# Optimization experiments

Measured on AMD Instinct MI355X. Metric: run time of the kernel, lower is better.

Reference implementation:

```python
import jax, jax.numpy as jnp
import numpy as np

EPS = 1e-5
LOSS_WEIGHT = 0.3
IGNORE_INDEX = -100


def rmsnorm(x, w):
    # x: (B,S,D), w: (D,)
    var = jnp.mean(x * x, axis=-1, keepdims=True)
    return x * jax.lax.rsqrt(var + EPS) * w


def cross_entropy(logits, targets):
    # logits: (B,T,V), targets: (B,T) int; ignore_index=-100, mean reduction
    logp = jax.nn.log_softmax(logits, axis=-1)
    valid = targets != IGNORE_INDEX
    safe_t = jnp.where(valid, targets, 0)
    nll = -jnp.take_along_axis(logp, safe_t[..., None], axis=-1)[..., 0]
    nll = jnp.where(valid, nll, 0.0)
    return jnp.sum(nll) / jnp.maximum(jnp.sum(valid), 1)


def setup_inputs() -> dict:
    key = jax.random.key(0)
    ks = jax.random.split(key, 5)
    B, S, D, V, H = 1, 2048, 1024, 50257, 3
    hidden = jax.random.normal(ks[0], (B, S, D), dtype=jnp.float32)
    targets = jax.random.randint(ks[1], (B, S), 0, V, dtype=jnp.int64)
    emb_w = jax.random.normal(ks[2], (V, D), dtype=jnp.float32) * 0.02
    main_norm_w = jnp.ones((D,), dtype=jnp.float32)
    aux_proj_w = jax.random.normal(ks[3], (H - 1, D, D), dtype=jnp.float32) * 0.02
    aux_norm_w = jnp.ones((H - 1, D), dtype=jnp.float32)
    aux_out_w = jax.random.normal(ks[4], (H - 1, V, D), dtype=jnp.float32) * 0.02
    return {"hidden": hidden, "targets": targets, "emb_w": emb_w,
            "main_norm_w": main_norm_w, "aux_proj_w": aux_proj_w,
            "aux_norm_w": aux_norm_w, "aux_out_w": aux_out_w}


def reference(hidden, targets, emb_w, main_norm_w, aux_proj_w, aux_norm_w, aux_out_w):
    # Main head: norm -> tied vocab projection
    main_logits = jnp.einsum('bsd,vd->bsv', rmsnorm(hidden, main_norm_w), emb_w)
    main_loss = cross_entropy(main_logits[:, :-1, :], targets[:, 1:])

    # Auxiliary heads predict t+2, t+3, ...
    n_aux = aux_proj_w.shape[0]
    aux_losses = []
    for i in range(n_aux):
        k = i + 2
        h = jnp.einsum('bsd,ed->bse', hidden, aux_proj_w[i])  # d_model -> d_model
        logits = jnp.einsum('bsd,vd->bsv', rmsnorm(h, aux_norm_w[i]), aux_out_w[i])
        aux_losses.append(cross_entropy(logits[:, :-k, :], targets[:, k:]))
    total_aux = sum(aux_losses) / len(aux_losses) if aux_losses else jnp.float32(0.0)
    loss = main_loss + LOSS_WEIGHT * total_aux
    return main_logits, loss
```

## Files before the change

kernel.cpp:

```cpp
#include <hip/hip_runtime.h>
#include <hip/hip_bf16.h>


typedef __hip_bfloat16 bf16;
typedef __attribute__((ext_vector_type(8))) short bf16x8;
typedef __attribute__((ext_vector_type(4))) float f32x4;

typedef const __attribute__((address_space(1))) void* gptr_t;
typedef __attribute__((address_space(3))) void* lptr_t;

#define S_LEN   2048
#define DMODEL  1024
#define VOCAB   50257
#define VPAD2   51200
#define NT256   200

__device__ __forceinline__ void gload_lds16(const void* g, void* l) {
  __builtin_amdgcn_global_load_lds((gptr_t)g, (lptr_t)l, 16, 0, 0);
}

__global__ __launch_bounds__(256) void k_cvt(const float* __restrict__ src,
                                             bf16* __restrict__ dst,
                                             long rows_src, long rows_pad) {
  const long total4 = rows_pad << 8;
  for (long i = (long)blockIdx.x * 256 + threadIdx.x; i < total4;
       i += (long)gridDim.x * 256) {
    const long e = i << 2;
    const long row = e >> 10;
    alignas(8) bf16 o[4];
    if (row < rows_src) {
      const float4 v = *(const float4*)(src + e);
      o[0] = __float2bfloat16(v.x); o[1] = __float2bfloat16(v.y);
      o[2] = __float2bfloat16(v.z); o[3] = __float2bfloat16(v.w);
    } else {
      o[0] = o[1] = o[2] = o[3] = __float2bfloat16(0.f);
    }
    *(uint2*)(dst + e) = *(const uint2*)o;
  }
}

__global__ __launch_bounds__(256) void k_rms(const float* __restrict__ x,
                                             const float* __restrict__ w,
                                             bf16* __restrict__ xn) {
  const int row = blockIdx.x;
  const int t = threadIdx.x;
  const float4 v = ((const float4*)(x + (size_t)row * DMODEL))[t];
  float ss = v.x*v.x + v.y*v.y + v.z*v.z + v.w*v.w;
  #pragma unroll
  for (int d = 1; d < 64; d <<= 1) ss += __shfl_xor(ss, d, 64);
  __shared__ float red[4];
  if ((t & 63) == 0) red[t >> 6] = ss;
  __syncthreads();
  const float tot = red[0] + red[1] + red[2] + red[3];
  const float scale = rsqrtf(tot * (1.f / DMODEL) + 1e-5f);
  const float4 wv = ((const float4*)w)[t];
  alignas(8) bf16 o[4];
  o[0] = __float2bfloat16(v.x * scale * wv.x);
  o[1] = __float2bfloat16(v.y * scale * wv.y);
  o[2] = __float2bfloat16(v.z * scale * wv.z);
  o[3] = __float2bfloat16(v.w * scale * wv.w);
  *(uint2*)(xn + (size_t)row * DMODEL + t * 4) = *(const uint2*)o;
}

template<bool WRITE_OUT, bool DO_CE>
__global__ __launch_bounds__(512, 2)
void k_gemm256(const bf16* __restrict__ A, const bf16* __restrict__ B,
               float* __restrict__ C, long ldc, int Nvalid,
               const int* __restrict__ targets, int shift,
               float* __restrict__ pmax, float* __restrict__ psum,
               float* __restrict__ ptgt, int ntiles) {
  __shared__ char lds[131072 + 9216];

  const int t = threadIdx.x;
  const int w = t >> 6, l = t & 63;
  const int g = l >> 4, q = l & 15;
  const int wr = w >> 2, wc = w & 3;
  const int id = blockIdx.x;
  const int bm = (id >> 3) & 7;
  const int bn = (id & 7) + ((id >> 6) << 3);

  f32x4 acc[8][4];
  #pragma unroll
  for (int i = 0; i < 8; ++i)
    #pragma unroll
    for (int j = 0; j < 4; ++j)
      #pragma unroll
      for (int r = 0; r < 4; ++r) acc[i][j][r] = 0.f;

  const int srow = (l >> 2);
  const int scol = ((l & 3) * 8) ^ (((l >> 5) & 1) * 16);
  const char* gA0 = (const char*)(A + (size_t)(bm * 256 + (w * 2 + 0) * 16 + srow) * DMODEL + scol);
  const char* gA1 = (const char*)(A + (size_t)(bm * 256 + (w * 2 + 1) * 16 + srow) * DMODEL + scol);
  const char* gB0 = (const char*)(B + (size_t)(bn * 256 + (w * 2 + 0) * 16 + srow) * DMODEL + scol);
  const char* gB1 = (const char*)(B + (size_t)(bn * 256 + (w * 2 + 1) * 16 + srow) * DMODEL + scol);

  const int laneoff = (q * 64 + g * 16) ^ (((q >> 3) & 1) << 5);
  const char* rdA = lds + wr * 8192 + laneoff;
  const char* rdB = lds + 16384 + wc * 4096 + laneoff;

#define RDA(BUF, KK, MI) (*(const bf16x8*)(rdA + (BUF)*65536 + (KK)*32768 + (MI)*1024))
#define RDB(BUF, KK, NI) (*(const bf16x8*)(rdB + (BUF)*65536 + (KK)*32768 + (NI)*1024))

#define STAGE(BUF, H, KOFF) do {                                                  \
    char* lb_ = lds + (BUF)*65536 + ((H)>>1)*32768 + ((H)&1)*16384 + w * 2048;    \
    const char* s0_ = ((H)&1) ? gB0 : gA0;                                        \
    const char* s1_ = ((H)&1) ? gB1 : gA1;                                        \
    gload_lds16(s0_ + (KOFF) + ((H)>>1)*64, lb_);                                 \
    gload_lds16(s1_ + (KOFF) + ((H)>>1)*64, lb_ + 1024);                          \
  } while (0)

#define PH_MFMA(MH)                                                               \
    __builtin_amdgcn_s_barrier();                                                 \
    __builtin_amdgcn_s_setprio(1);                                                \
    _Pragma("unroll")                                                             \
    for (int mi_ = 0; mi_ < 4; ++mi_)                                             \
      _Pragma("unroll")                                                           \
      for (int ni_ = 0; ni_ < 4; ++ni_)                                           \
        acc[(MH)*4 + mi_][ni_] = __builtin_amdgcn_mfma_f32_16x16x32_bf16(         \
            a[mi_], b[ni_], acc[(MH)*4 + mi_][ni_], 0, 0, 0);                     \
    __builtin_amdgcn_s_setprio(0);

#define TILE(BUF, DOSTG, KOFF, LAST) do {                                         \
    bf16x8 a[4], b[4];                                                            \
    _Pragma("unroll") for (int mi_ = 0; mi_ < 4; ++mi_) a[mi_] = RDA(BUF, 0, mi_);\
    _Pragma("unroll") for (int ni_ = 0; ni_ < 4; ++ni_) b[ni_] = RDB(BUF, 0, ni_);\
    if (DOSTG) STAGE(1-(BUF), 0, KOFF);                                           \
    PH_MFMA(0)                                                                    \
    __builtin_amdgcn_s_barrier();                                                 \
    _Pragma("unroll") for (int mi_ = 0; mi_ < 4; ++mi_) a[mi_] = RDA(BUF, 0, 4+mi_);\
    if (DOSTG) STAGE(1-(BUF), 1, KOFF);                                           \
    PH_MFMA(1)                                                                    \
    if (DOSTG) { asm volatile("s_waitcnt vmcnt(4)" ::: "memory"); }               \
    if (LAST)  { asm volatile("s_waitcnt vmcnt(0)" ::: "memory"); }               \
    __builtin_amdgcn_s_barrier();                                                 \
    _Pragma("unroll") for (int mi_ = 0; mi_ < 4; ++mi_) a[mi_] = RDA(BUF, 1, mi_);\
    _Pragma("unroll") for (int ni_ = 0; ni_ < 4; ++ni_) b[ni_] = RDB(BUF, 1, ni_);\
    if (DOSTG) STAGE(1-(BUF), 2, KOFF);                                           \
    PH_MFMA(0)                                                                    \
    __builtin_amdgcn_s_barrier();                                                 \
    _Pragma("unroll") for (int mi_ = 0; mi_ < 4; ++mi_) a[mi_] = RDA(BUF, 1, 4+mi_);\
    if (DOSTG) STAGE(1-(BUF), 3, KOFF);                                           \
    PH_MFMA(1)                                                                    \
    if (DOSTG) { asm volatile("s_waitcnt vmcnt(4)" ::: "memory"); }               \
    __builtin_amdgcn_s_barrier();                                                 \
  } while (0)

  STAGE(0, 0, 0); STAGE(0, 1, 0); STAGE(0, 2, 0); STAGE(0, 3, 0);
  asm volatile("s_waitcnt vmcnt(4)" ::: "memory");
  __builtin_amdgcn_s_barrier();

  for (int t2 = 0; t2 < 7; ++t2) {
    TILE(0, 1, 128, 0);
    TILE(1, 1, 256, 0);
    gA0 += 256; gA1 += 256; gB0 += 256; gB1 += 256;
  }
  TILE(0, 1, 128, 0);
  TILE(1, 0, 0, 1);

#undef TILE
#undef PH_MFMA
#undef STAGE
#undef RDA
#undef RDB

  if constexpr (WRITE_OUT) {
    #pragma unroll
    for (int mi = 0; mi < 8; ++mi) {
      #pragma unroll
      for (int r = 0; r < 4; ++r) {
        const long row = bm * 256 + wr * 128 + mi * 16 + g * 4 + r;
        #pragma unroll
        for (int ni = 0; ni < 4; ++ni) {
          const int col = bn * 256 + wc * 64 + ni * 16 + q;
          if (col < Nvalid) C[row * ldc + col] = acc[mi][ni][r];
        }
      }
    }
  }

  if constexpr (DO_CE) {
    float* lds_m = (float*)(lds + 131072);
    float* lds_s = lds_m + 1024;
    int* lds_tgt = (int*)(lds_s + 1024);
    if (t < 256) {
      const int rowg = bm * 256 + t;
      lds_tgt[t] = (rowg < S_LEN - shift) ? targets[rowg + shift] : -1;
    }
    __syncthreads();
    #pragma unroll
    for (int mi = 0; mi < 8; ++mi) {
      #pragma unroll
      for (int r = 0; r < 4; ++r) {
        const int rl = wr * 128 + mi * 16 + g * 4 + r;
        const int tgt = lds_tgt[rl];
        float v[4];
        #pragma unroll
        for (int ni = 0; ni < 4; ++ni) {
          const int n = bn * 256 + wc * 64 + ni * 16 + q;
          const float av = acc[mi][ni][r];
          if (n == tgt) ptgt[bm * 256 + rl] = av;
          v[ni] = (n < Nvalid) ? av : -1e30f;
        }
        float m = fmaxf(fmaxf(v[0], v[1]), fmaxf(v[2], v[3]));
        #pragma unroll
        for (int d = 1; d < 16; d <<= 1) m = fmaxf(m, __shfl_xor(m, d, 64));
        float s = 0.f;
        #pragma unroll
        for (int ni = 0; ni < 4; ++ni) s += __expf(v[ni] - m);
        #pragma unroll
        for (int d = 1; d < 16; d <<= 1) s += __shfl_xor(s, d, 64);
        if (q == 0) { lds_m[rl * 4 + wc] = m; lds_s[rl * 4 + wc] = s; }
      }
    }
    __syncthreads();
    if (t < 256) {
      float M = lds_m[t * 4 + 0], Ssum = lds_s[t * 4 + 0];
      #pragma unroll
      for (int c = 1; c < 4; ++c) {
        const float m2 = lds_m[t * 4 + c], s2 = lds_s[t * 4 + c];
        const float nM = fmaxf(M, m2);
        Ssum = Ssum * __expf(M - nM) + s2 * __expf(m2 - nM);
        M = nM;
      }
      const size_t idx = (size_t)(bm * 256 + t) * ntiles + bn;
      pmax[idx] = M;
      psum[idx] = Ssum;
    }
  }
}

__global__ __launch_bounds__(256, 2)
void k_gemm(const bf16* __restrict__ A, const bf16* __restrict__ B,
            float* __restrict__ C, long ldc, int Nvalid) {
  constexpr int K = DMODEL;
  __shared__ bf16 As[128 * 32];
  __shared__ bf16 Bs[128 * 32];

  const int t = threadIdx.x;
  const int bn = blockIdx.x, bm = blockIdx.y;
  const int w = t >> 6, l = t & 63, g = l >> 4, q = l & 15;
  const int wr = w >> 1, wc = w & 1;

  f32x4 acc[4][4];
  #pragma unroll
  for (int i = 0; i < 4; ++i)
    #pragma unroll
    for (int j = 0; j < 4; ++j)
      #pragma unroll
      for (int r = 0; r < 4; ++r) acc[i][j][r] = 0.f;

  char* lA0 = (char*)As + w * 1024;
  char* lA1 = (char*)As + 4096 + w * 1024;
  char* lB0 = (char*)Bs + w * 1024;
  char* lB1 = (char*)Bs + 4096 + w * 1024;
  const char* gA0 = (const char*)(A + (size_t)(bm * 128 + (t >> 2)) * K) + (t & 3) * 16;
  const char* gA1 = gA0 + (size_t)64 * K * 2;
  const char* gB0 = (const char*)(B + (size_t)(bn * 128 + (t >> 2)) * K) + (t & 3) * 16;
  const char* gB1 = gB0 + (size_t)64 * K * 2;

  for (int k0 = 0; k0 < K; k0 += 32) {
    const int kb = k0 * 2;
    gload_lds16(gA0 + kb, lA0);
    gload_lds16(gA1 + kb, lA1);
    gload_lds16(gB0 + kb, lB0);
    gload_lds16(gB1 + kb, lB1);
    __syncthreads();
    bf16x8 a[4], b[4];
    #pragma unroll
    for (int mi = 0; mi < 4; ++mi)
      a[mi] = *(const bf16x8*)&As[(wr * 64 + mi * 16 + q) * 32 + g * 8];
    #pragma unroll
    for (int ni = 0; ni < 4; ++ni)
      b[ni] = *(const bf16x8*)&Bs[(wc * 64 + ni * 16 + q) * 32 + g * 8];
    #pragma unroll
    for (int mi = 0; mi < 4; ++mi)
      #pragma unroll
      for (int ni = 0; ni < 4; ++ni)
        acc[mi][ni] = __builtin_amdgcn_mfma_f32_16x16x32_bf16(a[mi], b[ni], acc[mi][ni], 0, 0, 0);
    __syncthreads();
  }

  #pragma unroll
  for (int mi = 0; mi < 4; ++mi) {
    #pragma unroll
    for (int r = 0; r < 4; ++r) {
      const long row = bm * 128 + wr * 64 + mi * 16 + g * 4 + r;
      #pragma unroll
      for (int ni = 0; ni < 4; ++ni) {
        const int col = bn * 128 + wc * 64 + ni * 16 + q;
        if (col < Nvalid) C[row * ldc + col] = acc[mi][ni][r];
      }
    }
  }
}

__global__ __launch_bounds__(64) void k_combine(const float* __restrict__ pmax,
                                                const float* __restrict__ psum,
                                                const float* __restrict__ ptgt,
                                                float* __restrict__ nll,
                                                int ntiles, int nv) {
  const int r = blockIdx.x;
  const int l = threadIdx.x;
  float M = -1e30f, Ssum = 0.f;
  for (int tl = l; tl < ntiles; tl += 64) {
    const float m = pmax[(size_t)r * ntiles + tl];
    const float s = psum[(size_t)r * ntiles + tl];
    const float nM = fmaxf(M, m);
    Ssum = Ssum * __expf(M - nM) + s * __expf(m - nM);
    M = nM;
  }
  #pragma unroll
  for (int d = 1; d < 64; d <<= 1) {
    const float m2 = __shfl_xor(M, d, 64);
    const float s2 = __shfl_xor(Ssum, d, 64);
    const float nM = fmaxf(M, m2);
    Ssum = Ssum * __expf(M - nM) + s2 * __expf(m2 - nM);
    M = nM;
  }
  if (l == 0) nll[r] = (r < nv) ? (M + logf(Ssum) - ptgt[r]) : 0.f;
}

__global__ __launch_bounds__(256) void k_loss(const float* __restrict__ nll,
                                              float* __restrict__ out) {
  __shared__ float sh[256];
  const int t = threadIdx.x;
  float sums[3];
  #pragma unroll
  for (int h = 0; h < 3; ++h) {
    const int nv = 2047 - h;
    float s = 0.f;
    for (int r = t; r < nv; r += 256) s += nll[h * 2048 + r];
    sh[t] = s; __syncthreads();
    for (int off = 128; off > 0; off >>= 1) {
      if (t < off) sh[t] += sh[t + off];
      __syncthreads();
    }
    sums[h] = sh[0]; __syncthreads();
  }
  if (t == 0)
    out[0] = sums[0] / 2047.f + 0.3f * 0.5f * (sums[1] / 2046.f + sums[2] / 2045.f);
}

extern "C" void kernel_launch(void* const* d_in, const int* in_sizes, int n_in,
                              void* d_out, int out_size, void* d_ws, size_t ws_size,
                              hipStream_t stream) {
  const float* hidden      = (const float*)d_in[0];
  const int*   targets     = (const int*)d_in[1];
  const float* emb_w       = (const float*)d_in[2];
  const float* main_norm_w = (const float*)d_in[3];
  const float* aux_proj_w  = (const float*)d_in[4];
  const float* aux_norm_w  = (const float*)d_in[5];
  const float* aux_out_w   = (const float*)d_in[6];
  float* out = (float*)d_out;

  char* ws = (char*)d_ws;
  bf16*  Wb    = (bf16*)(ws);
  bf16*  hb    = (bf16*)(ws + 104857600);
  bf16*  xn    = (bf16*)(ws + 109051904);
  bf16*  projb = (bf16*)(ws + 113246208);
  float* hbuf  = (float*)(ws + 117440512);
  float* pmax  = (float*)(ws + 125829120);
  float* psum  = (float*)(ws + 127467520);
  float* ptgt  = (float*)(ws + 129105920);
  float* nll   = (float*)(ws + 129114112);

  k_cvt<<<2048, 256, 0, stream>>>(hidden, hb, 2048, 2048);
  k_cvt<<<2048, 256, 0, stream>>>(aux_proj_w, projb, 2048, 2048);
  k_rms<<<2048, 256, 0, stream>>>(hidden, main_norm_w, xn);

  k_cvt<<<2048, 256, 0, stream>>>(emb_w, Wb, VOCAB, VPAD2);
  k_gemm256<true, true><<<1600, 512, 0, stream>>>(
      xn, Wb, out, VOCAB, VOCAB, targets, 1, pmax, psum, ptgt, NT256);
  k_combine<<<2048, 64, 0, stream>>>(pmax, psum, ptgt, nll, NT256, 2047);

  for (int i = 0; i < 2; ++i) {
    k_cvt<<<2048, 256, 0, stream>>>(aux_out_w + (size_t)i * VOCAB * DMODEL, Wb, VOCAB, VPAD2);
    k_gemm<<<dim3(8, 16), 256, 0, stream>>>(
        hb, projb + (size_t)i * DMODEL * DMODEL, hbuf, DMODEL, DMODEL);
    k_rms<<<2048, 256, 0, stream>>>(hbuf, aux_norm_w + (size_t)i * DMODEL, xn);
    k_gemm256<false, true><<<1600, 512, 0, stream>>>(
        xn, Wb, nullptr, 0, VOCAB, targets, i + 2, pmax, psum, ptgt, NT256);
    k_combine<<<2048, 64, 0, stream>>>(pmax, psum, ptgt, nll + (i + 1) * 2048, NT256, 2048 - (i + 2));
  }

  k_loss<<<1, 256, 0, stream>>>(nll, out + (size_t)S_LEN * VOCAB);
}
```

Before: 1.205 ms.

## Replace double-buffered GEMM loop with multi-slot ring pipeline, per-head slot counts

```diff
diff --git a/kernel.cpp b/kernel.cpp
--- a/kernel.cpp
+++ b/kernel.cpp
@@ -62,14 +62,14 @@
   *(uint2*)(xn + (size_t)row * DMODEL + t * 4) = *(const uint2*)o;
 }
 
-template<bool WRITE_OUT, bool DO_CE>
+template<int SLOTS, bool WRITE_OUT, bool DO_CE>
 __global__ __launch_bounds__(512, 2)
 void k_gemm256(const bf16* __restrict__ A, const bf16* __restrict__ B,
                float* __restrict__ C, long ldc, int Nvalid,
                const int* __restrict__ targets, int shift,
                float* __restrict__ pmax, float* __restrict__ psum,
                float* __restrict__ ptgt, int ntiles) {
-  __shared__ char lds[131072 + 9216];
+  __shared__ char lds[SLOTS * 32768 + 9216];
 
   const int t = threadIdx.x;
   const int w = t >> 6, l = t & 63;
@@ -89,79 +89,83 @@
 
   const int srow = (l >> 2);
   const int scol = ((l & 3) * 8) ^ (((l >> 5) & 1) * 16);
-  const char* gA0 = (const char*)(A + (size_t)(bm * 256 + (w * 2 + 0) * 16 + srow) * DMODEL + scol);
-  const char* gA1 = (const char*)(A + (size_t)(bm * 256 + (w * 2 + 1) * 16 + srow) * DMODEL + scol);
-  const char* gB0 = (const char*)(B + (size_t)(bn * 256 + (w * 2 + 0) * 16 + srow) * DMODEL + scol);
-  const char* gB1 = (const char*)(B + (size_t)(bn * 256 + (w * 2 + 1) * 16 + srow) * DMODEL + scol);
+  const char* gA0 = (const char*)(A + (size_t)(bm * 256 + w * 32 + srow) * DMODEL + scol);
+  const char* gA1 = gA0 + (size_t)16 * DMODEL * 2;
+  const char* gB0 = (const char*)(B + (size_t)(bn * 256 + w * 32 + srow) * DMODEL + scol);
+  const char* gB1 = gB0 + (size_t)16 * DMODEL * 2;
 
   const int laneoff = (q * 64 + g * 16) ^ (((q >> 3) & 1) << 5);
   const char* rdA = lds + wr * 8192 + laneoff;
   const char* rdB = lds + 16384 + wc * 4096 + laneoff;
 
-#define RDA(BUF, KK, MI) (*(const bf16x8*)(rdA + (BUF)*65536 + (KK)*32768 + (MI)*1024))
-#define RDB(BUF, KK, NI) (*(const bf16x8*)(rdB + (BUF)*65536 + (KK)*32768 + (NI)*1024))
-
-#define STAGE(BUF, H, KOFF) do {                                                  \
-    char* lb_ = lds + (BUF)*65536 + ((H)>>1)*32768 + ((H)&1)*16384 + w * 2048;    \
-    const char* s0_ = ((H)&1) ? gB0 : gA0;                                        \
-    const char* s1_ = ((H)&1) ? gB1 : gA1;                                        \
-    gload_lds16(s0_ + (KOFF) + ((H)>>1)*64, lb_);                                 \
-    gload_lds16(s1_ + (KOFF) + ((H)>>1)*64, lb_ + 1024);                          \
-  } while (0)
-
-#define PH_MFMA(MH)                                                               \
-    __builtin_amdgcn_s_barrier();                                                 \
-    __builtin_amdgcn_s_setprio(1);                                                \
-    _Pragma("unroll")                                                             \
-    for (int mi_ = 0; mi_ < 4; ++mi_)                                             \
-      _Pragma("unroll")                                                           \
-      for (int ni_ = 0; ni_ < 4; ++ni_)                                           \
-        acc[(MH)*4 + mi_][ni_] = __builtin_amdgcn_mfma_f32_16x16x32_bf16(         \
-            a[mi_], b[ni_], acc[(MH)*4 + mi_][ni_], 0, 0, 0);                     \
+  auto lda = [&](int s, int mi) {
+    return *(const bf16x8*)(rdA + s * 32768 + mi * 1024);
+  };
+  auto ldb = [&](int s, int ni) {
+    return *(const bf16x8*)(rdB + s * 32768 + ni * 1024);
+  };
+  auto stageA = [&](int s, int koff) {
+    char* lb = lds + s * 32768 + w * 2048;
+    gload_lds16(gA0 + koff, lb);
+    gload_lds16(gA1 + koff, lb + 1024);
+  };
+  auto stageB = [&](int s, int koff) {
+    char* lb = lds + s * 32768 + 16384 + w * 2048;
+    gload_lds16(gB0 + koff, lb);
+    gload_lds16(gB1 + koff, lb + 1024);
+  };
+
+  #pragma unroll
+  for (int p = 0; p < SLOTS - 1; ++p) { stageA(p, p * 64); stageB(p, p * 64); }
+  if constexpr (SLOTS == 4) asm volatile("s_waitcnt vmcnt(8)" ::: "memory");
+  else if constexpr (SLOTS == 3) asm volatile("s_waitcnt vmcnt(4)" ::: "memory");
+  else asm volatile("s_waitcnt vmcnt(0)" ::: "memory");
+  __builtin_amdgcn_s_barrier();
+
+  #pragma unroll
+  for (int j = 0; j < 32; ++j) {
+    const int s = j % SLOTS;
+    const int sp = (j + SLOTS - 1) % SLOTS;
+    const int koff = (j + SLOTS - 1) * 64;
+    const bool do_stage = (j + SLOTS - 1) < 32;
+    bf16x8 a[4], b[4];
+
+    #pragma unroll
+    for (int mi = 0; mi < 4; ++mi) a[mi] = lda(s, mi);
+    #pragma unroll
+    for (int ni = 0; ni < 4; ++ni) b[ni] = ldb(s, ni);
+    if (do_stage) stageA(sp, koff);
+    __builtin_amdgcn_s_barrier();
+    __builtin_amdgcn_s_setprio(1);
+    #pragma unroll
+    for (int mi = 0; mi < 4; ++mi)
+      #pragma unroll
+      for (int ni = 0; ni < 4; ++ni)
+        acc[mi][ni] = __builtin_amdgcn_mfma_f32_16x16x32_bf16(a[mi], b[ni], acc[mi][ni], 0, 0, 0);
     __builtin_amdgcn_s_setprio(0);
-
-#define TILE(BUF, DOSTG, KOFF, LAST) do {                                         \
-    bf16x8 a[4], b[4];                                                            \
-    _Pragma("unroll") for (int mi_ = 0; mi_ < 4; ++mi_) a[mi_] = RDA(BUF, 0, mi_);\
-    _Pragma("unroll") for (int ni_ = 0; ni_ < 4; ++ni_) b[ni_] = RDB(BUF, 0, ni_);\
-    if (DOSTG) STAGE(1-(BUF), 0, KOFF);                                           \
-    PH_MFMA(0)                                                                    \
-    __builtin_amdgcn_s_barrier();                                                 \
-    _Pragma("unroll") for (int mi_ = 0; mi_ < 4; ++mi_) a[mi_] = RDA(BUF, 0, 4+mi_);\
-    if (DOSTG) STAGE(1-(BUF), 1, KOFF);                                           \
-    PH_MFMA(1)                                                                    \
-    if (DOSTG) { asm volatile("s_waitcnt vmcnt(4)" ::: "memory"); }               \
-    if (LAST)  { asm volatile("s_waitcnt vmcnt(0)" ::: "memory"); }               \
-    __builtin_amdgcn_s_barrier();                                                 \
-    _Pragma("unroll") for (int mi_ = 0; mi_ < 4; ++mi_) a[mi_] = RDA(BUF, 1, mi_);\
-    _Pragma("unroll") for (int ni_ = 0; ni_ < 4; ++ni_) b[ni_] = RDB(BUF, 1, ni_);\
-    if (DOSTG) STAGE(1-(BUF), 2, KOFF);                                           \
-    PH_MFMA(0)                                                                    \
-    __builtin_amdgcn_s_barrier();                                                 \
-    _Pragma("unroll") for (int mi_ = 0; mi_ < 4; ++mi_) a[mi_] = RDA(BUF, 1, 4+mi_);\
-    if (DOSTG) STAGE(1-(BUF), 3, KOFF);                                           \
-    PH_MFMA(1)                                                                    \
-    if (DOSTG) { asm volatile("s_waitcnt vmcnt(4)" ::: "memory"); }               \
-    __builtin_amdgcn_s_barrier();                                                 \
-  } while (0)
-
-  STAGE(0, 0, 0); STAGE(0, 1, 0); STAGE(0, 2, 0); STAGE(0, 3, 0);
-  asm volatile("s_waitcnt vmcnt(4)" ::: "memory");
-  __builtin_amdgcn_s_barrier();
-
-  for (int t2 = 0; t2 < 7; ++t2) {
-    TILE(0, 1, 128, 0);
-    TILE(1, 1, 256, 0);
-    gA0 += 256; gA1 += 256; gB0 += 256; gB1 += 256;
-  }
-  TILE(0, 1, 128, 0);
-  TILE(1, 0, 0, 1);
-
-#undef TILE
-#undef PH_MFMA
-#undef STAGE
-#undef RDA
-#undef RDB
+    __builtin_amdgcn_s_barrier();
+
+    #pragma unroll
+    for (int mi = 0; mi < 4; ++mi) a[mi] = lda(s, 4 + mi);
+    if (do_stage) stageB(sp, koff);
+    __builtin_amdgcn_s_barrier();
+    __builtin_amdgcn_s_setprio(1);
+    #pragma unroll
+    for (int mi = 0; mi < 4; ++mi)
+      #pragma unroll
+      for (int ni = 0; ni < 4; ++ni)
+        acc[4 + mi][ni] = __builtin_amdgcn_mfma_f32_16x16x32_bf16(a[mi], b[ni], acc[4 + mi][ni], 0, 0, 0);
+    __builtin_amdgcn_s_setprio(0);
+
+    if (j < 31) {
+      const int staged_hi = (j + SLOTS - 1 < 32) ? (j + SLOTS - 1) : 31;
+      const int nrem = 4 * (staged_hi - (j + 1));
+      if (nrem >= 8)      asm volatile("s_waitcnt vmcnt(8)" ::: "memory");
+      else if (nrem == 4) asm volatile("s_waitcnt vmcnt(4)" ::: "memory");
+      else                asm volatile("s_waitcnt vmcnt(0)" ::: "memory");
+    }
+    __builtin_amdgcn_s_barrier();
+  }
 
   if constexpr (WRITE_OUT) {
     #pragma unroll
@@ -179,7 +183,7 @@
   }
 
   if constexpr (DO_CE) {
-    float* lds_m = (float*)(lds + 131072);
+    float* lds_m = (float*)(lds + SLOTS * 32768);
     float* lds_s = lds_m + 1024;
     int* lds_tgt = (int*)(lds_s + 1024);
     if (t < 256) {
@@ -369,19 +373,24 @@
   k_rms<<<2048, 256, 0, stream>>>(hidden, main_norm_w, xn);
 
   k_cvt<<<2048, 256, 0, stream>>>(emb_w, Wb, VOCAB, VPAD2);
-  k_gemm256<true, true><<<1600, 512, 0, stream>>>(
+  k_gemm256<4, true, true><<<1600, 512, 0, stream>>>(
       xn, Wb, out, VOCAB, VOCAB, targets, 1, pmax, psum, ptgt, NT256);
   k_combine<<<2048, 64, 0, stream>>>(pmax, psum, ptgt, nll, NT256, 2047);
 
-  for (int i = 0; i < 2; ++i) {
-    k_cvt<<<2048, 256, 0, stream>>>(aux_out_w + (size_t)i * VOCAB * DMODEL, Wb, VOCAB, VPAD2);
-    k_gemm<<<dim3(8, 16), 256, 0, stream>>>(
-        hb, projb + (size_t)i * DMODEL * DMODEL, hbuf, DMODEL, DMODEL);
-    k_rms<<<2048, 256, 0, stream>>>(hbuf, aux_norm_w + (size_t)i * DMODEL, xn);
-    k_gemm256<false, true><<<1600, 512, 0, stream>>>(
-        xn, Wb, nullptr, 0, VOCAB, targets, i + 2, pmax, psum, ptgt, NT256);
-    k_combine<<<2048, 64, 0, stream>>>(pmax, psum, ptgt, nll + (i + 1) * 2048, NT256, 2048 - (i + 2));
-  }
+  k_cvt<<<2048, 256, 0, stream>>>(aux_out_w, Wb, VOCAB, VPAD2);
+  k_gemm<<<dim3(8, 16), 256, 0, stream>>>(hb, projb, hbuf, DMODEL, DMODEL);
+  k_rms<<<2048, 256, 0, stream>>>(hbuf, aux_norm_w, xn);
+  k_gemm256<3, false, true><<<1600, 512, 0, stream>>>(
+      xn, Wb, nullptr, 0, VOCAB, targets, 2, pmax, psum, ptgt, NT256);
+  k_combine<<<2048, 64, 0, stream>>>(pmax, psum, ptgt, nll + 2048, NT256, 2046);
+
+  k_cvt<<<2048, 256, 0, stream>>>(aux_out_w + (size_t)VOCAB * DMODEL, Wb, VOCAB, VPAD2);
+  k_gemm<<<dim3(8, 16), 256, 0, stream>>>(
+      hb, projb + (size_t)DMODEL * DMODEL, hbuf, DMODEL, DMODEL);
+  k_rms<<<2048, 256, 0, stream>>>(hbuf, aux_norm_w + DMODEL, xn);
+  k_gemm256<2, false, true><<<1600, 512, 0, stream>>>(
+      xn, Wb, nullptr, 0, VOCAB, targets, 3, pmax, psum, ptgt, NT256);
+  k_combine<<<2048, 64, 0, stream>>>(pmax, psum, ptgt, nll + 2 * 2048, NT256, 2045);
 
   k_loss<<<1, 256, 0, stream>>>(nll, out + (size_t)S_LEN * VOCAB);
 }
```

Result: slower. 1.337 ms (+10.9%).
